# Kernel optimization log

Measured on AMD Instinct MI355X. Metric: run time of the kernel, lower is better.

Reference implementation:

```python
import jax, jax.numpy as jnp
import numpy as np
import math

T = 32
DIM = 1024
BATCH = 4096
ETA = 1.0


def setup_inputs() -> dict:
    key = jax.random.key(0)
    k1, k2, k3, k4 = jax.random.split(key, 4)
    x = jax.random.normal(k1, (BATCH, DIM), dtype=jnp.float32)
    mu = jax.random.uniform(k2, (T, DIM), dtype=jnp.float32, minval=-0.5, maxval=0.5)
    rho = jax.random.uniform(k3, (T, DIM), dtype=jnp.float32, minval=-0.5, maxval=0.5)
    # stochastic Beta(gamma_1, gamma_2) draws in the original (scipy beta.rvs);
    # passed as an explicit input, kept strictly inside (0, 1)
    beta_samples = jax.random.uniform(k4, (BATCH, T), dtype=jnp.float32,
                                      minval=0.01, maxval=0.99)
    return {"x": x, "mu": mu, "rho": rho, "beta_samples": beta_samples}


def _forward(x, mu, rho, beta_samples):
    B, D = x.shape
    Tn = mu.shape[0]
    log2pi = math.log(2.0 * math.pi)

    std = jnp.log1p(jnp.exp(rho))              # [T, D]
    log_std_sum = jnp.sum(jnp.log(std), axis=-1)   # [T]
    inv_var = 1.0 / (std * std)                # [T, D]

    # Diagonal Gaussian log-prob, batched over all T components via GEMMs
    quad = (jnp.einsum('bd,td->bt', x * x, inv_var)
            - 2.0 * jnp.einsum('bd,td->bt', x, mu * inv_var)
            + jnp.sum(mu * mu * inv_var, axis=-1)[None, :])   # [B, T]
    log_pdfs = -0.5 * D * log2pi - log_std_sum[None, :] - 0.5 * quad  # [B, T]

    # entropy of each diagonal Gaussian, broadcast to batch
    entropy = (D / 2.0) * (log2pi + 1.0) + log_std_sum   # [T]
    entropy = jnp.broadcast_to(entropy[None, :], (B, Tn))

    # stick-breaking weights: pi = mix_weights(beta)[:, :-1]
    beta1m_cumprod = jnp.cumprod(1.0 - beta_samples, axis=-1)   # [B, T]
    pi = beta_samples * jnp.concatenate(
        [jnp.ones((B, 1), x.dtype), beta1m_cumprod[:, :-1]], axis=-1)  # [B, T]
    log_pi = jnp.log(pi)

    # get_phi
    kl_gaussian = log_pdfs + entropy            # [B, T]
    N_t_gaussian = jnp.sum(kl_gaussian, axis=0, keepdims=True)  # [1, T]
    N_t_pi = jnp.sum(log_pi, axis=0, keepdims=True)             # [1, T]
    mix = N_t_pi / (N_t_gaussian + N_t_pi)      # [1, T]
    kl = mix * kl_gaussian + (1.0 - mix) * log_pi
    phi_new = jax.nn.softmax(kl, axis=1)        # [B, T]
    kl_g_mixed = mix * kl_gaussian              # [B, T]

    likelihood = jnp.mean(jnp.sum(phi_new * kl_g_mixed, axis=1), axis=0)  # scalar
    return likelihood


def reference(x, mu, rho, beta_samples):
    return _forward(x, mu, rho, beta_samples)
```

## Files before the change

kernel.cpp:

```cpp
#include <hip/hip_runtime.h>
#include <math.h>

constexpr int NT = 32;
constexpr int ND = 1024;
constexpr int NB = 4096;
constexpr int NSLICE = 8;
constexpr int NRG   = 64;
constexpr int NBLK_MID = 256;

constexpr int OFF_M2C = 32768;
constexpr int OFF_C2  = 65536;
constexpr int OFF_KLG = 65600;
constexpr int OFF_LPI = 196672;
constexpr int OFF_QP  = 327744;
constexpr int OFF_PG  = 1376320;
constexpr int OFF_PP  = 1384512;

__global__ __launch_bounds__(256) void k_stats(const float* __restrict__ mu,
                                               const float* __restrict__ rho,
                                               float* __restrict__ ws,
                                               float* __restrict__ out) {
  float* ivc = ws;
  float* m2c = ws + OFF_M2C;
  float* c2  = ws + OFF_C2;

  const int t = blockIdx.x;
  const int c = threadIdx.x;

  float4 mu4  = reinterpret_cast<const float4*>(mu  + t * ND)[c];
  float4 rho4 = reinterpret_cast<const float4*>(rho + t * ND)[c];

  float rr[4] = {rho4.x, rho4.y, rho4.z, rho4.w};
  float mm[4] = {mu4.x,  mu4.y,  mu4.z,  mu4.w};
  float iv[4], m2[4];
  float c2p = 0.0f;
#pragma unroll
  for (int j = 0; j < 4; ++j) {
    float sd  = log1pf(expf(rr[j]));
    float ivv = 1.0f / (sd * sd);
    iv[j] = ivv;
    m2[j] = -2.0f * mm[j] * ivv;
    c2p  += mm[j] * mm[j] * ivv;
  }
  float4 iv4 = {iv[0], iv[1], iv[2], iv[3]};
  float4 m24 = {m2[0], m2[1], m2[2], m2[3]};
  reinterpret_cast<float4*>(ivc)[c * NT + t] = iv4;
  reinterpret_cast<float4*>(m2c)[c * NT + t] = m24;

#pragma unroll
  for (int m = 32; m >= 1; m >>= 1) c2p += __shfl_xor(c2p, m, 64);
  __shared__ float red[4];
  const int wave = threadIdx.x >> 6, lane = threadIdx.x & 63;
  if (lane == 0) red[wave] = c2p;
  __syncthreads();
  if (threadIdx.x == 0) {
    c2[t] = red[0] + red[1] + red[2] + red[3];
    if (t == 0) out[0] = 0.0f;
  }
}

__global__ __launch_bounds__(512, 4) void k_slice(const float* __restrict__ x,
                                                  float* __restrict__ ws) {
  float* qp = ws + OFF_QP;

  const int bid   = blockIdx.x;
  const int slice = bid >> 6;
  const int rg    = bid & 63;
  const int tid   = threadIdx.x;

  __shared__ float xs[64 * 128];
  __shared__ float ivs[32 * 32 * 4];
  __shared__ float m2s[32 * 32 * 4];

  {
    const float4* xg4 = reinterpret_cast<const float4*>(x);
    float4* xs4w = reinterpret_cast<float4*>(xs);
    const int row = tid >> 3;
    const int j0  = tid & 7;
#pragma unroll
    for (int p = 0; p < 4; ++p) {
      const int j = j0 + 8 * p;
      xs4w[row * 32 + j] =
          xg4[(size_t)(rg * 64 + row) * 256 + slice * 32 + j];
    }
  }
  {
    const float4* ivg = reinterpret_cast<const float4*>(ws) + (size_t)slice * 1024;
    const float4* m2g = reinterpret_cast<const float4*>(ws + OFF_M2C) + (size_t)slice * 1024;
    float4* ivw = reinterpret_cast<float4*>(ivs);
    float4* m2w = reinterpret_cast<float4*>(m2s);
    ivw[tid]       = ivg[tid];
    ivw[tid + 512] = ivg[tid + 512];
    m2w[tid]       = m2g[tid];
    m2w[tid + 512] = m2g[tid + 512];
  }
  __syncthreads();

  const int q    = tid >> 6;
  const int lane = tid & 63;
  const int h = lane >> 5, t = lane & 31;
  const float4* ivs4 = reinterpret_cast<const float4*>(ivs);
  const float4* m2s4 = reinterpret_cast<const float4*>(m2s);
  const float4* xsr  = reinterpret_cast<const float4*>(xs) + (size_t)(q * 8) * 32;

  float a[8] = {0.f, 0.f, 0.f, 0.f, 0.f, 0.f, 0.f, 0.f};
#pragma unroll 2
  for (int i = 0; i < 16; ++i) {
    const int c = h * 16 + i;
    float4 iv4 = ivs4[c * 32 + t];
    float4 m24 = m2s4[c * 32 + t];
#pragma unroll
    for (int r = 0; r < 8; ++r) {
      float4 xv = xsr[r * 32 + c];
      a[r] = fmaf(xv.x, fmaf(xv.x, iv4.x, m24.x), a[r]);
      a[r] = fmaf(xv.y, fmaf(xv.y, iv4.y, m24.y), a[r]);
      a[r] = fmaf(xv.z, fmaf(xv.z, iv4.z, m24.z), a[r]);
      a[r] = fmaf(xv.w, fmaf(xv.w, iv4.w, m24.w), a[r]);
    }
  }
#pragma unroll
  for (int r = 0; r < 8; ++r) a[r] += __shfl_xor(a[r], 32, 64);

  if (h == 0) {
#pragma unroll
    for (int r = 0; r < 8; ++r) {
      const int row = rg * 64 + q * 8 + r;
      qp[((size_t)slice * NB + row) * NT + t] = a[r];
    }
  }
}

__global__ __launch_bounds__(512) void k_mid(const float* __restrict__ beta,
                                             float* __restrict__ ws) {
  const float* c2 = ws + OFF_C2;
  const float* qp = ws + OFF_QP;
  float* klg = ws + OFF_KLG;
  float* lpi = ws + OFF_LPI;
  float* Pg  = ws + OFF_PG;
  float* Pp  = ws + OFF_PP;

  const int tid = threadIdx.x;
  const int rr = tid >> 5, t = tid & 31;
  const int row = blockIdx.x * 16 + rr;

  float quad = 0.f;
#pragma unroll
  for (int s = 0; s < NSLICE; ++s)
    quad += qp[((size_t)s * NB + row) * NT + t];

  const float kv = 512.0f - 0.5f * (quad + c2[t]);
  klg[(size_t)row * NT + t] = kv;

  const float b = beta[(size_t)row * NT + t];
  const float l1m = log1pf(-b);
  float s = l1m;
#pragma unroll
  for (int d = 1; d < 32; d <<= 1) {
    float v = __shfl_up(s, (unsigned)d, 32);
    if (t >= d) s += v;
  }
  const float lp = logf(b) + (s - l1m);
  lpi[(size_t)row * NT + t] = lp;

  __shared__ float klP[16][32], lpP[16][32];
  klP[rr][t] = kv;
  lpP[rr][t] = lp;
  __syncthreads();
  if (tid < 32) {
    float sg = 0.f, sp = 0.f;
#pragma unroll
    for (int r = 0; r < 16; ++r) { sg += klP[r][tid]; sp += lpP[r][tid]; }
    Pg[(size_t)blockIdx.x * NT + tid] = sg;
    Pp[(size_t)blockIdx.x * NT + tid] = sp;
  }
}

__global__ __launch_bounds__(512) void k_final(const float* __restrict__ ws,
                                               float* __restrict__ out) {
  const float* klg = ws + OFF_KLG;
  const float* lpi = ws + OFF_LPI;
  const float* Pg  = ws + OFF_PG;
  const float* Pp  = ws + OFF_PP;

  const int tid  = threadIdx.x;
  const int wave = tid >> 6, lane = tid & 63;
  const int t = tid & 31;
  const int g = tid >> 5;

  __shared__ float ngF[32], npF[32];
  __shared__ float redG[8][32], redP[8][32];
  __shared__ float red[8];

  {
    float sg = 0.f, sp = 0.f;
#pragma unroll 4
    for (int b = g; b < NBLK_MID; b += 16) {
      sg += Pg[(size_t)b * NT + t];
      sp += Pp[(size_t)b * NT + t];
    }
    sg += __shfl_xor(sg, 32, 64);
    sp += __shfl_xor(sp, 32, 64);
    if (lane < 32) { redG[wave][t] = sg; redP[wave][t] = sp; }
  }
  __syncthreads();
  if (tid < 32) {
    float ng = 0.f, np = 0.f;
#pragma unroll
    for (int w = 0; w < 8; ++w) { ng += redG[w][tid]; np += redP[w][tid]; }
    ngF[tid] = ng;
    npF[tid] = np;
  }
  __syncthreads();

  const int row = blockIdx.x * 16 + g;
  const float kg = klg[(size_t)row * NT + t];
  const float lp = lpi[(size_t)row * NT + t];
  const float ng = ngF[t], np = npF[t];
  const float mix  = np / (ng + np);
  const float klgm = mix * kg;
  const float kl   = klgm + (1.0f - mix) * lp;

  float m = kl;
#pragma unroll
  for (int mk = 16; mk >= 1; mk >>= 1) m = fmaxf(m, __shfl_xor(m, mk, 64));
  const float e = expf(kl - m);
  float num = e * klgm, den = e;
#pragma unroll
  for (int mk = 16; mk >= 1; mk >>= 1) {
    num += __shfl_xor(num, mk, 64);
    den += __shfl_xor(den, mk, 64);
  }
  float s = num / den;
  s += __shfl_xor(s, 32, 64);

  if (lane == 0) red[wave] = s;
  __syncthreads();
  if (tid == 0) {
    float tot = 0.f;
#pragma unroll
    for (int w = 0; w < 8; ++w) tot += red[w];
    atomicAdd(out, tot * (1.0f / (float)NB));
  }
}

extern "C" void kernel_launch(void* const* d_in, const int* in_sizes, int n_in,
                              void* d_out, int out_size, void* d_ws, size_t ws_size,
                              hipStream_t stream) {
  const float* x    = (const float*)d_in[0];
  const float* mu   = (const float*)d_in[1];
  const float* rho  = (const float*)d_in[2];
  const float* beta = (const float*)d_in[3];
  float* out = (float*)d_out;
  float* ws  = (float*)d_ws;

  hipLaunchKernelGGL(k_stats, dim3(32),  dim3(256), 0, stream, mu, rho, ws, out);
  hipLaunchKernelGGL(k_slice, dim3(NSLICE * NRG), dim3(512), 0, stream, x, ws);
  hipLaunchKernelGGL(k_mid,   dim3(NBLK_MID), dim3(512), 0, stream, beta, ws);
  hipLaunchKernelGGL(k_final, dim3(256), dim3(512), 0, stream, ws, out);
}
```

Baseline: 31.09 us.

## Fuse stats kernel into slice kernel and split D into 16 slices

Removes the separate k_stats launch: each k_slice block now computes inv_var and -2*mu*inv_var for its own D-slice directly from mu and rho, and blocks with rg==0 write per-slice partial c2 sums into an extra row of the partial-quad buffer. The D dimension is split into 16 slices instead of 8, which doubles the block count to 1024 and halves shared memory per block, with occupancy hints raised to 8. The intent is to drop one kernel launch and improve parallelism. In exchange, the softplus math is recomputed redundantly in every row-group block and k_mid must read twice as many partial sums.

New measurement: 34.06 us. 1.1x slower.

```diff
diff --git a/kernel.cpp b/kernel.cpp
--- a/kernel.cpp
+++ b/kernel.cpp
@@ -4,62 +4,19 @@
 constexpr int NT = 32;
 constexpr int ND = 1024;
 constexpr int NB = 4096;
-constexpr int NSLICE = 8;
-constexpr int NRG   = 64;
+constexpr int NSLICE = 16;
+constexpr int NRG    = 64;
+constexpr int QROWS  = NB + 1;
 constexpr int NBLK_MID = 256;
 
-constexpr int OFF_M2C = 32768;
-constexpr int OFF_C2  = 65536;
-constexpr int OFF_KLG = 65600;
-constexpr int OFF_LPI = 196672;
-constexpr int OFF_QP  = 327744;
-constexpr int OFF_PG  = 1376320;
-constexpr int OFF_PP  = 1384512;
-
-__global__ __launch_bounds__(256) void k_stats(const float* __restrict__ mu,
-                                               const float* __restrict__ rho,
-                                               float* __restrict__ ws,
-                                               float* __restrict__ out) {
-  float* ivc = ws;
-  float* m2c = ws + OFF_M2C;
-  float* c2  = ws + OFF_C2;
-
-  const int t = blockIdx.x;
-  const int c = threadIdx.x;
-
-  float4 mu4  = reinterpret_cast<const float4*>(mu  + t * ND)[c];
-  float4 rho4 = reinterpret_cast<const float4*>(rho + t * ND)[c];
-
-  float rr[4] = {rho4.x, rho4.y, rho4.z, rho4.w};
-  float mm[4] = {mu4.x,  mu4.y,  mu4.z,  mu4.w};
-  float iv[4], m2[4];
-  float c2p = 0.0f;
-#pragma unroll
-  for (int j = 0; j < 4; ++j) {
-    float sd  = log1pf(expf(rr[j]));
-    float ivv = 1.0f / (sd * sd);
-    iv[j] = ivv;
-    m2[j] = -2.0f * mm[j] * ivv;
-    c2p  += mm[j] * mm[j] * ivv;
-  }
-  float4 iv4 = {iv[0], iv[1], iv[2], iv[3]};
-  float4 m24 = {m2[0], m2[1], m2[2], m2[3]};
-  reinterpret_cast<float4*>(ivc)[c * NT + t] = iv4;
-  reinterpret_cast<float4*>(m2c)[c * NT + t] = m24;
-
-#pragma unroll
-  for (int m = 32; m >= 1; m >>= 1) c2p += __shfl_xor(c2p, m, 64);
-  __shared__ float red[4];
-  const int wave = threadIdx.x >> 6, lane = threadIdx.x & 63;
-  if (lane == 0) red[wave] = c2p;
-  __syncthreads();
-  if (threadIdx.x == 0) {
-    c2[t] = red[0] + red[1] + red[2] + red[3];
-    if (t == 0) out[0] = 0.0f;
-  }
-}
-
-__global__ __launch_bounds__(512, 4) void k_slice(const float* __restrict__ x,
+constexpr int OFF_LPI = 131072;
+constexpr int OFF_QP  = 262144;
+constexpr int OFF_PG  = 2359808;
+constexpr int OFF_PP  = 2368000;
+
+__global__ __launch_bounds__(512, 8) void k_slice(const float* __restrict__ x,
+                                                  const float* __restrict__ mu,
+                                                  const float* __restrict__ rho,
                                                   float* __restrict__ ws) {
   float* qp = ws + OFF_QP;
 
@@ -68,31 +25,50 @@
   const int rg    = bid & 63;
   const int tid   = threadIdx.x;
 
-  __shared__ float xs[64 * 128];
-  __shared__ float ivs[32 * 32 * 4];
-  __shared__ float m2s[32 * 32 * 4];
+  __shared__ float xs[64 * 64];
+  __shared__ float ivs[16 * 32 * 4];
+  __shared__ float m2s[16 * 32 * 4];
+
+  float c2p4 = 0.0f;
+  {
+    const int t  = tid >> 4;
+    const int c4 = tid & 15;
+    const float4* mug = reinterpret_cast<const float4*>(mu);
+    const float4* rhg = reinterpret_cast<const float4*>(rho);
+    float4 mu4 = mug[(size_t)t * 256 + slice * 16 + c4];
+    float4 rh4 = rhg[(size_t)t * 256 + slice * 16 + c4];
+    float mm[4] = {mu4.x, mu4.y, mu4.z, mu4.w};
+    float rr[4] = {rh4.x, rh4.y, rh4.z, rh4.w};
+    float iv[4], m2[4];
+#pragma unroll
+    for (int j = 0; j < 4; ++j) {
+      float sd  = log1pf(expf(rr[j]));
+      float ivv = 1.0f / (sd * sd);
+      iv[j] = ivv;
+      m2[j] = -2.0f * mm[j] * ivv;
+      c2p4 += mm[j] * mm[j] * ivv;
+    }
+    reinterpret_cast<float4*>(ivs)[c4 * 32 + t] = {iv[0], iv[1], iv[2], iv[3]};
+    reinterpret_cast<float4*>(m2s)[c4 * 32 + t] = {m2[0], m2[1], m2[2], m2[3]};
+  }
 
   {
     const float4* xg4 = reinterpret_cast<const float4*>(x);
     float4* xs4w = reinterpret_cast<float4*>(xs);
     const int row = tid >> 3;
     const int j0  = tid & 7;
-#pragma unroll
-    for (int p = 0; p < 4; ++p) {
-      const int j = j0 + 8 * p;
-      xs4w[row * 32 + j] =
-          xg4[(size_t)(rg * 64 + row) * 256 + slice * 32 + j];
-    }
-  }
-  {
-    const float4* ivg = reinterpret_cast<const float4*>(ws) + (size_t)slice * 1024;
-    const float4* m2g = reinterpret_cast<const float4*>(ws + OFF_M2C) + (size_t)slice * 1024;
-    float4* ivw = reinterpret_cast<float4*>(ivs);
-    float4* m2w = reinterpret_cast<float4*>(m2s);
-    ivw[tid]       = ivg[tid];
-    ivw[tid + 512] = ivg[tid + 512];
-    m2w[tid]       = m2g[tid];
-    m2w[tid + 512] = m2g[tid + 512];
+    xs4w[row * 16 + j0]     = xg4[(size_t)(rg * 64 + row) * 256 + slice * 16 + j0];
+    xs4w[row * 16 + j0 + 8] = xg4[(size_t)(rg * 64 + row) * 256 + slice * 16 + j0 + 8];
+  }
+
+  if (rg == 0) {
+    float s = c2p4;
+#pragma unroll
+    for (int mk = 1; mk < 16; mk <<= 1) s += __shfl_xor(s, mk, 64);
+    if ((tid & 15) == 0) {
+      const int t = tid >> 4;
+      qp[((size_t)slice * QROWS + NB) * NT + t] = s;
+    }
   }
   __syncthreads();
 
@@ -101,17 +77,17 @@
   const int h = lane >> 5, t = lane & 31;
   const float4* ivs4 = reinterpret_cast<const float4*>(ivs);
   const float4* m2s4 = reinterpret_cast<const float4*>(m2s);
-  const float4* xsr  = reinterpret_cast<const float4*>(xs) + (size_t)(q * 8) * 32;
+  const float4* xsr  = reinterpret_cast<const float4*>(xs) + (size_t)(q * 8) * 16;
 
   float a[8] = {0.f, 0.f, 0.f, 0.f, 0.f, 0.f, 0.f, 0.f};
-#pragma unroll 2
-  for (int i = 0; i < 16; ++i) {
-    const int c = h * 16 + i;
+#pragma unroll
+  for (int i = 0; i < 8; ++i) {
+    const int c = h * 8 + i;
     float4 iv4 = ivs4[c * 32 + t];
     float4 m24 = m2s4[c * 32 + t];
 #pragma unroll
     for (int r = 0; r < 8; ++r) {
-      float4 xv = xsr[r * 32 + c];
+      float4 xv = xsr[r * 16 + c];
       a[r] = fmaf(xv.x, fmaf(xv.x, iv4.x, m24.x), a[r]);
       a[r] = fmaf(xv.y, fmaf(xv.y, iv4.y, m24.y), a[r]);
       a[r] = fmaf(xv.z, fmaf(xv.z, iv4.z, m24.z), a[r]);
@@ -125,16 +101,16 @@
 #pragma unroll
     for (int r = 0; r < 8; ++r) {
       const int row = rg * 64 + q * 8 + r;
-      qp[((size_t)slice * NB + row) * NT + t] = a[r];
+      qp[((size_t)slice * QROWS + row) * NT + t] = a[r];
     }
   }
 }
 
 __global__ __launch_bounds__(512) void k_mid(const float* __restrict__ beta,
-                                             float* __restrict__ ws) {
-  const float* c2 = ws + OFF_C2;
+                                             float* __restrict__ ws,
+                                             float* __restrict__ out) {
   const float* qp = ws + OFF_QP;
-  float* klg = ws + OFF_KLG;
+  float* klg = ws;
   float* lpi = ws + OFF_LPI;
   float* Pg  = ws + OFF_PG;
   float* Pp  = ws + OFF_PP;
@@ -143,12 +119,16 @@
   const int rr = tid >> 5, t = tid & 31;
   const int row = blockIdx.x * 16 + rr;
 
-  float quad = 0.f;
-#pragma unroll
-  for (int s = 0; s < NSLICE; ++s)
-    quad += qp[((size_t)s * NB + row) * NT + t];
-
-  const float kv = 512.0f - 0.5f * (quad + c2[t]);
+  if (blockIdx.x == 0 && tid == 0) out[0] = 0.0f;
+
+  float quad = 0.f, c2t = 0.f;
+#pragma unroll
+  for (int s = 0; s < NSLICE; ++s) {
+    quad += qp[((size_t)s * QROWS + row) * NT + t];
+    c2t  += qp[((size_t)s * QROWS + NB) * NT + t];
+  }
+
+  const float kv = 512.0f - 0.5f * (quad + c2t);
   klg[(size_t)row * NT + t] = kv;
 
   const float b = beta[(size_t)row * NT + t];
@@ -177,7 +157,7 @@
 
 __global__ __launch_bounds__(512) void k_final(const float* __restrict__ ws,
                                                float* __restrict__ out) {
-  const float* klg = ws + OFF_KLG;
+  const float* klg = ws;
   const float* lpi = ws + OFF_LPI;
   const float* Pg  = ws + OFF_PG;
   const float* Pp  = ws + OFF_PP;
@@ -253,8 +233,9 @@
   float* out = (float*)d_out;
   float* ws  = (float*)d_ws;
 
-  hipLaunchKernelGGL(k_stats, dim3(32),  dim3(256), 0, stream, mu, rho, ws, out);
-  hipLaunchKernelGGL(k_slice, dim3(NSLICE * NRG), dim3(512), 0, stream, x, ws);
-  hipLaunchKernelGGL(k_mid,   dim3(NBLK_MID), dim3(512), 0, stream, beta, ws);
+  hipLaunchKernelGGL(k_slice, dim3(NSLICE * NRG), dim3(512), 0, stream,
+                     x, mu, rho, ws);
+  hipLaunchKernelGGL(k_mid,   dim3(NBLK_MID), dim3(512), 0, stream,
+                     beta, ws, out);
   hipLaunchKernelGGL(k_final, dim3(256), dim3(512), 0, stream, ws, out);
 }
```
